# Kernel optimization log

Measured on AMD Instinct MI355X. Metric: run time of the kernel, lower is better.

The kernel has to match this reference:

```python
import jax, jax.numpy as jnp
import numpy as np

POOL = 7  # pool_size
R = 1024  # num_rois
H = W = 128
C = 512


def setup_inputs() -> dict:
    key = jax.random.key(0)
    k1, k2, k3, k4, k5 = jax.random.split(key, 5)
    feature_map = jax.random.normal(k1, (1, H, W, C), dtype=jnp.float32)
    # rois layout per source: [xmin, xmax, ymin, ymax], integer-valued floats, xmax>xmin, ymax>ymin
    xmin = jax.random.randint(k2, (R,), 0, W - 33)
    ymin = jax.random.randint(k3, (R,), 0, H - 33)
    wdt = jax.random.randint(k4, (R,), 2, 32)
    hgt = jax.random.randint(k5, (R,), 2, 32)
    rois = jnp.stack([xmin, xmin + wdt, ymin, ymin + hgt], axis=1).astype(jnp.float32)
    return {"feature_map": feature_map, "rois": rois}


def _axis_coords(lo, size, pool):
    # Legacy TF1 tf.image.resize_images (bilinear, align_corners=False):
    #   src = dst * (in_size / out_size); i0 = floor(src); i1 = min(i0+1, in_size-1)
    scale = size.astype(jnp.float32) / pool                     # [R]
    src = jnp.arange(pool, dtype=jnp.float32)[None, :] * scale[:, None]  # [R,P]
    i0 = jnp.floor(src).astype(jnp.int32)
    i1 = jnp.minimum(i0 + 1, size[:, None] - 1)
    frac = src - i0.astype(jnp.float32)
    return lo[:, None] + i0, lo[:, None] + i1, frac             # global indices, lerp weights


def reference(feature_map, rois):
    fm = feature_map[0]                                  # [H,W,C]
    ri = rois.astype(jnp.int32)
    xmin, xmax, ymin, ymax = ri[:, 0], ri[:, 1], ri[:, 2], ri[:, 3]
    y0, y1, fy = _axis_coords(ymin, ymax - ymin, POOL)   # [R,P] each
    x0, x1, fx = _axis_coords(xmin, xmax - xmin, POOL)
    # Fused gather + bilinear sample: one pass over the full feature map.
    tl = fm[y0[:, :, None], x0[:, None, :]]              # [R,P,P,C]
    tr = fm[y0[:, :, None], x1[:, None, :]]
    bl = fm[y1[:, :, None], x0[:, None, :]]
    br = fm[y1[:, :, None], x1[:, None, :]]
    fx_ = fx[:, None, :, None]                           # [R,1,P,1]
    fy_ = fy[:, :, None, None]                           # [R,P,1,1]
    top = tl + (tr - tl) * fx_
    bot = bl + (br - bl) * fx_
    return top + (bot - top) * fy_                       # [R,P,P,C]
```

## Files before the change

### kernel.cpp

```cpp
#include <hip/hip_runtime.h>

#define POOL 7
#define FM_H 128
#define FM_W 128
#define FM_C 512
#define NGRP 8
#define GRP_C (FM_C / NGRP)
#define CELLS_PER_BLK 16

typedef float f32x4 __attribute__((ext_vector_type(4)));

__global__ __launch_bounds__(256) void roi_pool_kernel(
    const float* __restrict__ fm,
    const float* __restrict__ rois,
    float* __restrict__ out,
    int n_cells)
{
    const int tid  = threadIdx.x;
    const int g    = blockIdx.x & (NGRP - 1);
    const int cb   = blockIdx.x >> 3;
    const int cell = cb * CELLS_PER_BLK + (tid >> 4);
    if (cell >= n_cells) return;
    const int c4   = (g << 6) + ((tid & 15) << 2);

    const int r  = cell / (POOL * POOL);
    const int p  = cell - r * (POOL * POOL);
    const int py = p / POOL;
    const int px = p - py * POOL;

    const float4 rv = *reinterpret_cast<const float4*>(rois + (size_t)r * 4);
    const int xmin = (int)rv.x;
    const int xmax = (int)rv.y;
    const int ymin = (int)rv.z;
    const int ymax = (int)rv.w;
    const int sy = ymax - ymin;
    const int sx = xmax - xmin;

    const float scy  = (float)sy / 7.0f;
    const float srcy = (float)py * scy;
    const int   iy0  = (int)floorf(srcy);
    const int   iy1  = min(iy0 + 1, sy - 1);
    const float fy   = srcy - (float)iy0;
    const int   y0   = ymin + iy0;
    const int   y1   = ymin + iy1;

    const float scx  = (float)sx / 7.0f;
    const float srcx = (float)px * scx;
    const int   ix0  = (int)floorf(srcx);
    const int   ix1  = min(ix0 + 1, sx - 1);
    const float fx   = srcx - (float)ix0;
    const int   x0   = xmin + ix0;
    const int   x1   = xmin + ix1;

    const size_t o00 = ((size_t)(y0 * FM_W + x0)) * FM_C + c4;
    const size_t o01 = ((size_t)(y0 * FM_W + x1)) * FM_C + c4;
    const size_t o10 = ((size_t)(y1 * FM_W + x0)) * FM_C + c4;
    const size_t o11 = ((size_t)(y1 * FM_W + x1)) * FM_C + c4;

    const float4 tl = *reinterpret_cast<const float4*>(fm + o00);
    const float4 tr = *reinterpret_cast<const float4*>(fm + o01);
    const float4 bl = *reinterpret_cast<const float4*>(fm + o10);
    const float4 br = *reinterpret_cast<const float4*>(fm + o11);

    f32x4 o;
    {
        float top, bot;
        top = tl.x + (tr.x - tl.x) * fx; bot = bl.x + (br.x - bl.x) * fx; o.x = top + (bot - top) * fy;
        top = tl.y + (tr.y - tl.y) * fx; bot = bl.y + (br.y - bl.y) * fx; o.y = top + (bot - top) * fy;
        top = tl.z + (tr.z - tl.z) * fx; bot = bl.z + (br.z - bl.z) * fx; o.z = top + (bot - top) * fy;
        top = tl.w + (tr.w - tl.w) * fx; bot = bl.w + (br.w - bl.w) * fx; o.w = top + (bot - top) * fy;
    }

    f32x4* dst = reinterpret_cast<f32x4*>(out + (size_t)cell * FM_C + c4);
    __builtin_nontemporal_store(o, dst);
}

extern "C" void kernel_launch(void* const* d_in, const int* in_sizes, int n_in,
                              void* d_out, int out_size, void* d_ws, size_t ws_size,
                              hipStream_t stream) {
    const float* fm   = (const float*)d_in[0];
    const float* rois = (const float*)d_in[1];
    float* out        = (float*)d_out;

    const int R       = in_sizes[1] / 4;
    const int n_cells = R * POOL * POOL;
    const int cblocks = (n_cells + CELLS_PER_BLK - 1) / CELLS_PER_BLK;
    const int blocks  = cblocks * NGRP;

    roi_pool_kernel<<<blocks, 256, 0, stream>>>(fm, rois, out, n_cells);
}
```

Baseline: 27.49 us.

## Bin ROI rows by feature-map stripe to localize gathers per XCD

Adds a binning pass that buckets each (roi, pool-row) task by which 16-row stripe of the feature map it samples, using atomics into a workspace list. The main kernel then interleaves blocks across eight stripes, so that under round-robin block-to-XCD dispatch each XCD's L2 serves one stripe. Each block now handles a whole pool row across all channels instead of a channel slice of 16 cells. This adds a memset and an extra kernel launch, over-launches blocks that exit early, and keeps the old kernel as a fallback when the workspace is too small.

```diff
diff --git a/kernel.cpp b/kernel.cpp
--- a/kernel.cpp
+++ b/kernel.cpp
@@ -4,29 +4,49 @@
 #define FM_H 128
 #define FM_W 128
 #define FM_C 512
-#define NGRP 8
-#define GRP_C (FM_C / NGRP)
+#define NSTRIPE 8
 #define CELLS_PER_BLK 16
 
 typedef float f32x4 __attribute__((ext_vector_type(4)));
 
-__global__ __launch_bounds__(256) void roi_pool_kernel(
+__global__ __launch_bounds__(256) void bin_kernel(
+    const float* __restrict__ rois, int* __restrict__ count,
+    int* __restrict__ list, int n_tasks, int cap)
+{
+    const int t = blockIdx.x * 256 + threadIdx.x;
+    if (t >= n_tasks) return;
+    const int r  = t / POOL;
+    const int py = t - r * POOL;
+
+    const float4 rv = *reinterpret_cast<const float4*>(rois + (size_t)r * 4);
+    const int ymin = (int)rv.z;
+    const int ymax = (int)rv.w;
+    const int sy   = ymax - ymin;
+
+    const float scy  = (float)sy / 7.0f;
+    const float srcy = (float)py * scy;
+    const int   iy0  = (int)floorf(srcy);
+    const int   y0   = ymin + iy0;
+
+    const int s   = y0 >> 4;
+    const int pos = atomicAdd(&count[s], 1);
+    list[s * cap + pos] = t;
+}
+
+__global__ __launch_bounds__(256) void pool_stripe_kernel(
     const float* __restrict__ fm,
     const float* __restrict__ rois,
     float* __restrict__ out,
-    int n_cells)
+    const int* __restrict__ count,
+    const int* __restrict__ list,
+    int cap)
 {
-    const int tid  = threadIdx.x;
-    const int g    = blockIdx.x & (NGRP - 1);
-    const int cb   = blockIdx.x >> 3;
-    const int cell = cb * CELLS_PER_BLK + (tid >> 4);
-    if (cell >= n_cells) return;
-    const int c4   = (g << 6) + ((tid & 15) << 2);
-
-    const int r  = cell / (POOL * POOL);
-    const int p  = cell - r * (POOL * POOL);
-    const int py = p / POOL;
-    const int px = p - py * POOL;
+    const int s = blockIdx.x & (NSTRIPE - 1);
+    const int i = blockIdx.x >> 3;
+    if (i >= count[s]) return;
+    const int t  = list[s * cap + i];
+    const int r  = t / POOL;
+    const int py = t - r * POOL;
 
     const float4 rv = *reinterpret_cast<const float4*>(rois + (size_t)r * 4);
     const int xmin = (int)rv.x;
@@ -44,32 +64,88 @@
     const int   y0   = ymin + iy0;
     const int   y1   = ymin + iy1;
 
-    const float scx  = (float)sx / 7.0f;
-    const float srcx = (float)px * scx;
-    const int   ix0  = (int)floorf(srcx);
-    const int   ix1  = min(ix0 + 1, sx - 1);
-    const float fx   = srcx - (float)ix0;
-    const int   x0   = xmin + ix0;
-    const int   x1   = xmin + ix1;
+    const float scx = (float)sx / 7.0f;
 
-    const size_t o00 = ((size_t)(y0 * FM_W + x0)) * FM_C + c4;
-    const size_t o01 = ((size_t)(y0 * FM_W + x1)) * FM_C + c4;
-    const size_t o10 = ((size_t)(y1 * FM_W + x0)) * FM_C + c4;
-    const size_t o11 = ((size_t)(y1 * FM_W + x1)) * FM_C + c4;
+    const int half = threadIdx.x >> 7;
+    const int lane = threadIdx.x & 127;
+    const int c4   = lane << 2;
 
-    const float4 tl = *reinterpret_cast<const float4*>(fm + o00);
-    const float4 tr = *reinterpret_cast<const float4*>(fm + o01);
-    const float4 bl = *reinterpret_cast<const float4*>(fm + o10);
-    const float4 br = *reinterpret_cast<const float4*>(fm + o11);
+    const size_t rowy0 = (size_t)y0 * FM_W;
+    const size_t rowy1 = (size_t)y1 * FM_W;
+    const size_t obase = ((size_t)t) * POOL * FM_C;
+
+    #pragma unroll
+    for (int j = 0; j < 4; ++j) {
+        const int px = j * 2 + half;
+        if (px < POOL) {
+            const float srcx = (float)px * scx;
+            const int   ix0  = (int)floorf(srcx);
+            const int   ix1  = min(ix0 + 1, sx - 1);
+            const float fx   = srcx - (float)ix0;
+            const int   x0   = xmin + ix0;
+            const int   x1   = xmin + ix1;
+
+            const float4 tl = *reinterpret_cast<const float4*>(fm + (rowy0 + x0) * FM_C + c4);
+            const float4 tr = *reinterpret_cast<const float4*>(fm + (rowy0 + x1) * FM_C + c4);
+            const float4 bl = *reinterpret_cast<const float4*>(fm + (rowy1 + x0) * FM_C + c4);
+            const float4 br = *reinterpret_cast<const float4*>(fm + (rowy1 + x1) * FM_C + c4);
+
+            f32x4 o;
+            {
+                float top, bot;
+                top = tl.x + (tr.x - tl.x) * fx; bot = bl.x + (br.x - bl.x) * fx; o.x = top + (bot - top) * fy;
+                top = tl.y + (tr.y - tl.y) * fx; bot = bl.y + (br.y - bl.y) * fx; o.y = top + (bot - top) * fy;
+                top = tl.z + (tr.z - tl.z) * fx; bot = bl.z + (br.z - bl.z) * fx; o.z = top + (bot - top) * fy;
+                top = tl.w + (tr.w - tl.w) * fx; bot = bl.w + (br.w - bl.w) * fx; o.w = top + (bot - top) * fy;
+            }
+
+            f32x4* dst = reinterpret_cast<f32x4*>(out + obase + (size_t)px * FM_C + c4);
+            __builtin_nontemporal_store(o, dst);
+        }
+    }
+}
+
+__global__ __launch_bounds__(256) void roi_pool_fallback(
+    const float* __restrict__ fm, const float* __restrict__ rois,
+    float* __restrict__ out, int n_cells)
+{
+    const int tid  = threadIdx.x;
+    const int g    = blockIdx.x & 7;
+    const int cb   = blockIdx.x >> 3;
+    const int cell = cb * CELLS_PER_BLK + (tid >> 4);
+    if (cell >= n_cells) return;
+    const int c4   = (g << 6) + ((tid & 15) << 2);
+
+    const int r  = cell / (POOL * POOL);
+    const int p  = cell - r * (POOL * POOL);
+    const int py = p / POOL;
+    const int px = p - py * POOL;
+
+    const float4 rv = *reinterpret_cast<const float4*>(rois + (size_t)r * 4);
+    const int xmin = (int)rv.x, xmax = (int)rv.y, ymin = (int)rv.z, ymax = (int)rv.w;
+    const int sy = ymax - ymin, sx = xmax - xmin;
+
+    const float scy = (float)sy / 7.0f, srcy = (float)py * scy;
+    const int iy0 = (int)floorf(srcy), iy1 = min(iy0 + 1, sy - 1);
+    const float fy = srcy - (float)iy0;
+    const int y0 = ymin + iy0, y1 = ymin + iy1;
+
+    const float scx = (float)sx / 7.0f, srcx = (float)px * scx;
+    const int ix0 = (int)floorf(srcx), ix1 = min(ix0 + 1, sx - 1);
+    const float fx = srcx - (float)ix0;
+    const int x0 = xmin + ix0, x1 = xmin + ix1;
+
+    const float4 tl = *reinterpret_cast<const float4*>(fm + ((size_t)(y0 * FM_W + x0)) * FM_C + c4);
+    const float4 tr = *reinterpret_cast<const float4*>(fm + ((size_t)(y0 * FM_W + x1)) * FM_C + c4);
+    const float4 bl = *reinterpret_cast<const float4*>(fm + ((size_t)(y1 * FM_W + x0)) * FM_C + c4);
+    const float4 br = *reinterpret_cast<const float4*>(fm + ((size_t)(y1 * FM_W + x1)) * FM_C + c4);
 
     f32x4 o;
-    {
-        float top, bot;
-        top = tl.x + (tr.x - tl.x) * fx; bot = bl.x + (br.x - bl.x) * fx; o.x = top + (bot - top) * fy;
-        top = tl.y + (tr.y - tl.y) * fx; bot = bl.y + (br.y - bl.y) * fx; o.y = top + (bot - top) * fy;
-        top = tl.z + (tr.z - tl.z) * fx; bot = bl.z + (br.z - bl.z) * fx; o.z = top + (bot - top) * fy;
-        top = tl.w + (tr.w - tl.w) * fx; bot = bl.w + (br.w - bl.w) * fx; o.w = top + (bot - top) * fy;
-    }
+    float top, bot;
+    top = tl.x + (tr.x - tl.x) * fx; bot = bl.x + (br.x - bl.x) * fx; o.x = top + (bot - top) * fy;
+    top = tl.y + (tr.y - tl.y) * fx; bot = bl.y + (br.y - bl.y) * fx; o.y = top + (bot - top) * fy;
+    top = tl.z + (tr.z - tl.z) * fx; bot = bl.z + (br.z - bl.z) * fx; o.z = top + (bot - top) * fy;
+    top = tl.w + (tr.w - tl.w) * fx; bot = bl.w + (br.w - bl.w) * fx; o.w = top + (bot - top) * fy;
 
     f32x4* dst = reinterpret_cast<f32x4*>(out + (size_t)cell * FM_C + c4);
     __builtin_nontemporal_store(o, dst);
@@ -83,9 +159,21 @@
     float* out        = (float*)d_out;
 
     const int R       = in_sizes[1] / 4;
-    const int n_cells = R * POOL * POOL;
-    const int cblocks = (n_cells + CELLS_PER_BLK - 1) / CELLS_PER_BLK;
-    const int blocks  = cblocks * NGRP;
+    const int n_tasks = R * POOL;
+    const int cap     = n_tasks;
+    const size_t need = (size_t)NSTRIPE * 4 + (size_t)NSTRIPE * cap * 4;
 
-    roi_pool_kernel<<<blocks, 256, 0, stream>>>(fm, rois, out, n_cells);
+    if (ws_size < need) {
+        const int n_cells = R * POOL * POOL;
+        const int cblocks = (n_cells + CELLS_PER_BLK - 1) / CELLS_PER_BLK;
+        roi_pool_fallback<<<cblocks * 8, 256, 0, stream>>>(fm, rois, out, n_cells);
+        return;
+    }
+
+    int* count = (int*)d_ws;
+    int* list  = count + NSTRIPE;
+
+    hipMemsetAsync(count, 0, NSTRIPE * sizeof(int), stream);
+    bin_kernel<<<(n_tasks + 255) / 256, 256, 0, stream>>>(rois, count, list, n_tasks, cap);
+    pool_stripe_kernel<<<n_tasks * NSTRIPE, 256, 0, stream>>>(fm, rois, out, count, list, cap);
 }
```

After: 94.50 us. +243.8%, slower.
